# Performance work log

Hardware: AMD Instinct MI355X
Metric: run time of the kernel (lower is better)

## Reference

```python
import jax, jax.numpy as jnp
import numpy as np

N_NODES = 10000
N_EDGES = 5_000_000
BATCH = 2000


def setup_inputs() -> dict:
    key = jax.random.key(0)
    k1, k2, k3, k4 = jax.random.split(key, 4)
    n, E = N_NODES, N_EDGES
    # valid undirected pairs i < j
    i = jax.random.randint(k1, (E,), 0, n - 1)
    r = jax.random.randint(k2, (E,), 0, n)
    j = i + 1 + r % (n - 1 - i)
    edges = jnp.stack([i, j])  # [2, E], int
    edge_times = jax.random.uniform(k3, (E,), dtype=jnp.float32)
    edge_states = jax.random.randint(k4, (E,), 0, 2)
    return {
        "edges": edges,
        "edge_times": edge_times,
        "edge_states": edge_states,
        "nodes_num": n,
        "batch_size": BATCH,
    }


def _flat_idx(i, j, n):
    # undirected upper-triangular linearization of pair (i, j), i < j
    return i * n - i * (i + 1) // 2 + (j - i - 1)


def reference(edges, edge_times, edge_states, nodes_num, batch_size):
    n = nodes_num
    # -- multinomial(arange(n), batch_size, replacement=False) via Gumbel top-k --
    key = jax.random.key(19)
    w = jnp.arange(n, dtype=jnp.float32)
    logw = jnp.where(w > 0, jnp.log(jnp.maximum(w, 1.0)), -jnp.inf)
    scores = logw + jax.random.gumbel(key, (n,), dtype=jnp.float32)
    _, sel = jax.lax.top_k(scores, batch_size)
    batch_nodes = jnp.sort(sel)

    # -- all combinations (i < j since batch_nodes is sorted) --
    ii, jj = np.triu_indices(batch_size, k=1)  # static shapes
    batch_pairs = jnp.stack([batch_nodes[ii], batch_nodes[jj]])  # [2, P]
    batch_flat = _flat_idx(batch_pairs[0], batch_pairs[1], n)  # ascending

    # -- gather stored edges whose pair index is in the batch --
    edge_flat = _flat_idx(edges[0], edges[1], n)
    order = jnp.argsort(edge_flat)  # jax sort is stable -> matches coalesce order
    edges_sorted = edges[:, order]
    flat_sorted = edge_flat[order]
    times_sorted = edge_times[order]
    states_sorted = edge_states[order]

    pos = jnp.searchsorted(batch_flat, flat_sorted)
    pos = jnp.clip(pos, 0, batch_flat.shape[0] - 1)
    mask = batch_flat[pos] == flat_sorted  # [E] membership of each edge in batch

    batch_edge_times = jnp.where(mask, times_sorted, 0.0)
    batch_states = jnp.where(mask, states_sorted, 0)
    return (batch_nodes, batch_pairs, edges_sorted, batch_edge_times,
            batch_states, mask)
```

## Files before the change

### kernel.cpp

```cpp
#include <hip/hip_runtime.h>
#include <stdint.h>
#include <math.h>

#define N_NODES  10000
#define N_EDGES  5000000
#define BATCH    2000
#define N_PAIRS  1999000

#define OUT_BN      0
#define OUT_PAIRS0  2000
#define OUT_PAIRS1  2001000
#define OUT_ES0     4000000
#define OUT_ES1     9000000
#define OUT_T       14000000
#define OUT_S       19000000
#define OUT_M       24000000

#define WS_KEYS     0
#define WS_SEL      80000
#define WS_BN       120000
#define WS_CNT      128000
#define WS_FILL     168000
#define WS_OFF      208000
#define WS_SCRATCH  248064


#define RPB_LOG  7
#define NB1      79
#define CHUNK    4096
#define NBIN     192
#define NBITSW   313
#define RANK_BLKS 200
#define HIST_BLKS 128

typedef unsigned long long u64;

__device__ __forceinline__ u64 score_key(int w, unsigned bits) {
  const float TINY = 1.17549435e-38f;
  float uf = __uint_as_float((bits >> 9) | 0x3f800000u) - 1.0f;
  float val = fmaxf(TINY, uf + TINY);
  float t1 = (float)log((double)val);
  float gmb = -(float)log((double)(-t1));
  float score = (w > 0) ? ((float)log((double)w) + gmb) : (-INFINITY);
  unsigned fb = __float_as_uint(score);
  unsigned s = (fb & 0x80000000u) ? ~fb : (fb | 0x80000000u);
  unsigned d = ~s;
  return ((u64)d << 32) | (unsigned)w;
}

__device__ __forceinline__ u64 make_key(int v) {
  unsigned ks[3] = {0u, 19u, 0u ^ 19u ^ 0x1BD11BDAu};
  unsigned x0 = 0u + ks[0];
  unsigned x1 = (unsigned)v + ks[1];
  const int R0[4] = {13, 15, 26, 6};
  const int R1[4] = {17, 29, 16, 24};
#pragma unroll
  for (int g = 0; g < 5; ++g) {
    const int* R = (g & 1) ? R1 : R0;
#pragma unroll
    for (int r = 0; r < 4; ++r) {
      x0 += x1;
      x1 = (x1 << R[r]) | (x1 >> (32 - R[r]));
      x1 ^= x0;
    }
    x0 += ks[(g + 1) % 3];
    x1 += ks[(g + 2) % 3] + (unsigned)(g + 1);
  }
  return score_key(v, x0 ^ x1);
}

__global__ void __launch_bounds__(256) k_rankhist(
    int* __restrict__ rankc, int* __restrict__ cnt,
    const int4* __restrict__ e_i4) {
  __shared__ __align__(16) int sh4[N_NODES];
  int tid = threadIdx.x;
  if ((int)blockIdx.x < RANK_BLKS) {
    u64* lk = (u64*)sh4;
    int vblk = blockIdx.x / 5, cblk = blockIdx.x % 5;
    int base = cblk * 2048;
    int lenc = min(2048, N_NODES - base);
    for (int t = tid; t < lenc; t += 256) lk[t] = make_key(base + t);
    __syncthreads();
    int v = vblk * 256 + tid;
    u64 kv = (v < N_NODES) ? make_key(v) : 0;
    int c = 0;
    for (int t = 0; t < lenc; ++t) c += (lk[t] < kv) ? 1 : 0;
    if (v < N_NODES && c) atomicAdd(&rankc[v], c);
  } else {
    int* h = sh4;
    for (int t = tid; t < N_NODES; t += 256) h[t] = 0;
    __syncthreads();
    int hb = blockIdx.x - RANK_BLKS;
    int stride = HIST_BLKS * 256;
    for (int t = hb * 256 + tid; t < N_EDGES / 4; t += stride) {
      int4 r = e_i4[t];
      atomicAdd(&h[r.x], 1);
      atomicAdd(&h[r.y], 1);
      atomicAdd(&h[r.z], 1);
      atomicAdd(&h[r.w], 1);
    }
    __syncthreads();
    for (int t = tid; t < N_NODES; t += 256) {
      int c = h[t];
      if (c) atomicAdd(&cnt[t], c);
    }
  }
}

__global__ void k_scan_all(const int* rankc, int* sel, int* bn, float* outbn,
                           const int* cnt, int* off, int* fill, int* fill1,
                           unsigned* selbits) {
  __shared__ int wsum[16];
  __shared__ unsigned lb[320];
  const int PER = 10;
  int tid = threadIdx.x, lane = tid & 63, wid = tid >> 6;
  int base = tid * PER;
  int svv[PER];
  {
    int s = 0;
#pragma unroll
    for (int k = 0; k < PER; ++k) {
      int i = base + k;
      if (i < N_NODES) {
        int sv = (rankc[i] < BATCH) ? 1 : 0;
        sel[i] = sv;
        svv[k] = sv;
        s += sv;
      } else svv[k] = 0;
    }
    int inc = s;
#pragma unroll
    for (int d = 1; d < 64; d <<= 1) {
      int v = __shfl_up(inc, d, 64);
      if (lane >= d) inc += v;
    }
    if (lane == 63) wsum[wid] = inc;
    __syncthreads();
    int woff = 0;
    for (int w = 0; w < wid; ++w) woff += wsum[w];
    int run = woff + inc - s;
#pragma unroll
    for (int k = 0; k < PER; ++k) {
      int i = base + k;
      if (i < N_NODES && svv[k]) {
        bn[run] = i;
        outbn[run] = (float)i;
        ++run;
      }
    }
  }
  __syncthreads();
  {
    int cv[PER];
    int s = 0;
#pragma unroll
    for (int k = 0; k < PER; ++k) {
      int i = base + k;
      if (i < N_NODES) { cv[k] = cnt[i]; s += cv[k]; } else cv[k] = 0;
    }
    int inc = s;
#pragma unroll
    for (int d = 1; d < 64; d <<= 1) {
      int v = __shfl_up(inc, d, 64);
      if (lane >= d) inc += v;
    }
    if (lane == 63) wsum[wid] = inc;
    __syncthreads();
    int woff = 0;
    for (int w = 0; w < wid; ++w) woff += wsum[w];
    int run = woff + inc - s;
#pragma unroll
    for (int k = 0; k < PER; ++k) {
      int i = base + k;
      if (i < N_NODES) {
        off[i] = run;
        fill[i] = run;
        if ((i & ((1 << RPB_LOG) - 1)) == 0) fill1[i >> RPB_LOG] = run;
        run += cv[k];
      }
    }
    if (tid == 0) off[N_NODES] = N_EDGES;
  }
  __syncthreads();
  if (tid < 320) lb[tid] = 0;
  __syncthreads();
#pragma unroll
  for (int k = 0; k < PER; ++k) {
    int i = base + k;
    if (i < N_NODES && svv[k]) atomicOr(&lb[i >> 5], 1u << (i & 31));
  }
  __syncthreads();
  if (tid < NBITSW) selbits[tid] = lb[tid];
}

__global__ void __launch_bounds__(256) k_pairs_part1(
    const int* __restrict__ e_i, const int* __restrict__ e_j,
    const int* __restrict__ st, int* __restrict__ fill1,
    u64* __restrict__ stage, const int* __restrict__ bn,
    float* __restrict__ outp, int nblk1) {
  __shared__ u64 lkey[CHUNK];
  __shared__ int h[NB1], bstart[NB1], basec[NB1], cur[NB1];
  __shared__ int tcount_s;
  int tid = threadIdx.x;
  if ((int)blockIdx.x >= nblk1) {
    int p = ((int)blockIdx.x - nblk1) * 256 + tid;
    if (p >= N_PAIRS) return;
    float tf = 2.0f * BATCH - 1.0f;
    float disc = tf * tf - 8.0f * (float)p;
    int ii = (int)((tf - sqrtf(disc)) * 0.5f);
    if (ii < 0) ii = 0;
    if (ii > BATCH - 2) ii = BATCH - 2;
    while (ii > 0 &&
           (long long)ii * (BATCH - 1) - (long long)ii * (ii - 1) / 2 > p) --ii;
    while ((long long)(ii + 1) * (BATCH - 1) - (long long)(ii + 1) * ii / 2 <= p) ++ii;
    long long S = (long long)ii * (BATCH - 1) - (long long)ii * (ii - 1) / 2;
    int jj = ii + 1 + (int)(p - S);
    outp[p] = (float)bn[ii];
    outp[N_PAIRS + p] = (float)bn[jj];
    return;
  }
  int c0 = (int)blockIdx.x * CHUNK;
  int nloc = min(CHUNK, N_EDGES - c0);
  for (int t = tid; t < NB1; t += 256) h[t] = 0;
  __syncthreads();
  int iv[CHUNK / 256];
  const int4* e_i4 = (const int4*)(e_i + c0);
#pragma unroll
  for (int k = 0; k < CHUNK / 1024; ++k) {
    int q = tid + 256 * k;
    int ebase = 4 * q;
    if (ebase < nloc) {
      int4 r = e_i4[q];
      iv[4 * k + 0] = r.x; iv[4 * k + 1] = r.y;
      iv[4 * k + 2] = r.z; iv[4 * k + 3] = r.w;
      atomicAdd(&h[r.x >> RPB_LOG], 1);
      atomicAdd(&h[r.y >> RPB_LOG], 1);
      atomicAdd(&h[r.z >> RPB_LOG], 1);
      atomicAdd(&h[r.w >> RPB_LOG], 1);
    } else {
      iv[4 * k + 0] = iv[4 * k + 1] = iv[4 * k + 2] = iv[4 * k + 3] = -1;
    }
  }
  __syncthreads();
  if (tid < 64) {
    int a = h[tid];
    int b = (tid + 64 < NB1) ? h[tid + 64] : 0;
    int inc0 = a;
#pragma unroll
    for (int d = 1; d < 64; d <<= 1) {
      int v = __shfl_up(inc0, d, 64);
      if (tid >= d) inc0 += v;
    }
    int t0 = __shfl(inc0, 63, 64);
    int inc1 = b;
#pragma unroll
    for (int d = 1; d < 64; d <<= 1) {
      int v = __shfl_up(inc1, d, 64);
      if (tid >= d) inc1 += v;
    }
    int tot = t0 + __shfl(inc1, 63, 64);
    bstart[tid] = inc0 - a;
    if (tid + 64 < NB1) bstart[tid + 64] = t0 + inc1 - b;
    if (tid == 0) tcount_s = tot;
  }
  __syncthreads();
  for (int b = tid; b < NB1; b += 256) {
    basec[b] = h[b] ? atomicAdd(&fill1[b], h[b]) : 0;
    cur[b] = bstart[b];
  }
  __syncthreads();
  const int4* e_j4 = (const int4*)(e_j + c0);
  const int4* st4 = (const int4*)(st + c0);
#pragma unroll
  for (int k = 0; k < CHUNK / 1024; ++k) {
    int q = tid + 256 * k;
    int ebase = 4 * q;
    if (ebase < nloc) {
      int4 jj = e_j4[q];
      int4 ss = st4[q];
      int js[4] = {jj.x, jj.y, jj.z, jj.w};
      int s4[4] = {ss.x, ss.y, ss.z, ss.w};
#pragma unroll
      for (int c = 0; c < 4; ++c) {
        int i = iv[4 * k + c];
        unsigned e = (unsigned)(c0 + ebase + c);
        int b = i >> RPB_LOG;
        int pos = atomicAdd(&cur[b], 1);
        lkey[pos] = ((u64)(unsigned)i << 38) | ((u64)(unsigned)js[c] << 24) |
                    ((u64)e << 1) | (u64)(unsigned)s4[c];
      }
    }
  }
  __syncthreads();
  int tcount = tcount_s;
  for (int t = tid; t < tcount; t += 256) {
    u64 kv = lkey[t];
    int b = (int)(kv >> (38 + RPB_LOG));
    stage[basec[b] + (t - bstart[b])] = kv;
  }
}

__global__ void __launch_bounds__(256) k_part2(
    const u64* __restrict__ stage, int* __restrict__ fill,
    u64* __restrict__ sk) {
  __shared__ u64 lkey[CHUNK];
  __shared__ int h[256], bstart[256], baser[256], cur[256], wsum4[4];
  __shared__ int rowbase_s;
  int tid = threadIdx.x, lane = tid & 63, wid = tid >> 6;
  int c0 = (int)blockIdx.x * CHUNK;
  int nloc = min(CHUNK, N_EDGES - c0);
  h[tid] = 0;
  if (tid == 0)
    rowbase_s = ((int)(stage[c0] >> (38 + RPB_LOG))) << RPB_LOG;
  __syncthreads();
  int rowbase = rowbase_s;
  u64 kv[CHUNK / 256];
#pragma unroll
  for (int k = 0; k < CHUNK / 256; ++k) {
    int q = tid + 256 * k;
    if (q < nloc) {
      kv[k] = stage[c0 + q];
      atomicAdd(&h[(int)(kv[k] >> 38) - rowbase], 1);
    }
  }
  __syncthreads();
  int hv = h[tid];
  int inc = hv;
#pragma unroll
  for (int d = 1; d < 64; d <<= 1) {
    int v = __shfl_up(inc, d, 64);
    if (lane >= d) inc += v;
  }
  if (lane == 63) wsum4[wid] = inc;
  __syncthreads();
  int woff = 0;
  for (int w = 0; w < wid; ++w) woff += wsum4[w];
  int tcount = wsum4[0] + wsum4[1] + wsum4[2] + wsum4[3];
  int excl = woff + inc - hv;
  bstart[tid] = excl;
  cur[tid] = excl;
  baser[tid] = hv ? atomicAdd(&fill[rowbase + tid], hv) : 0;
  __syncthreads();
#pragma unroll
  for (int k = 0; k < CHUNK / 256; ++k) {
    int q = tid + 256 * k;
    if (q < nloc) {
      int lr = (int)(kv[k] >> 38) - rowbase;
      int pos = atomicAdd(&cur[lr], 1);
      lkey[pos] = kv[k];
    }
  }
  __syncthreads();
  for (int t = tid; t < tcount; t += 256) {
    u64 v = lkey[t];
    int lr = (int)(v >> 38) - rowbase;
    sk[baser[lr] + (t - bstart[lr])] = v;
  }
}

__global__ void __launch_bounds__(256) k_rowsort_key(
    const u64* __restrict__ sk, const int* __restrict__ off,
    const float* __restrict__ times, const unsigned* __restrict__ selbits,
    float* __restrict__ out) {
  __shared__ u64 buf[768];
  __shared__ int hist[NBIN], cur[NBIN];
  __shared__ unsigned bits[320];
  int tid = threadIdx.x;
  int row = blockIdx.x;
  int o0 = off[row], o1 = off[row + 1];
  int len = o1 - o0;
  if (len <= 0) return;
  if (len > 768) len = 768;
  int span = N_NODES - 1 - row;
  int s = 0;
  while ((span >> s) >= 160) ++s;
  int mi = (int)((selbits[row >> 5] >> (row & 31)) & 1u);
  for (int t = tid; t < NBIN; t += 256) hist[t] = 0;
  if (mi) {
    for (int t = tid; t < NBITSW; t += 256) bits[t] = selbits[t];
  }
  __syncthreads();
  u64 kv[3];
  int dv[3], rv[3];
  int jbase = row + 1;
#pragma unroll
  for (int k = 0; k < 3; ++k) {
    int t = tid + 256 * k;
    if (t < len) {
      u64 v = sk[o0 + t];
      kv[k] = v;
      int j = (int)((v >> 24) & 0x3FFFull);
      int d = (j - jbase) >> s;
      dv[k] = d;
      atomicAdd(&hist[d], 1);
    } else {
      dv[k] = -1;
    }
  }
  __syncthreads();
  if (tid < 64) {
    int b0 = tid * 3;
    int c0 = hist[b0], c1 = hist[b0 + 1], c2 = hist[b0 + 2];
    int sum = c0 + c1 + c2;
    int inc = sum;
#pragma unroll
    for (int d = 1; d < 64; d <<= 1) {
      int v = __shfl_up(inc, d, 64);
      if (tid >= d) inc += v;
    }
    int excl = inc - sum;
    hist[b0] = excl;
    hist[b0 + 1] = excl + c0;
    hist[b0 + 2] = excl + c0 + c1;
    cur[b0] = excl;
    cur[b0 + 1] = excl + c0;
    cur[b0 + 2] = excl + c0 + c1;
  }
  __syncthreads();
#pragma unroll
  for (int k = 0; k < 3; ++k) {
    if (dv[k] >= 0) {
      int pos = atomicAdd(&cur[dv[k]], 1);
      buf[pos] = kv[k];
    }
  }
  __syncthreads();
#pragma unroll
  for (int k = 0; k < 3; ++k) {
    if (dv[k] >= 0) {
      u64 me = kv[k];
      int s0 = hist[dv[k]];
      int s1 = cur[dv[k]];
      int r = 0;
      for (int q = s0; q < s1; ++q) r += (buf[q] < me) ? 1 : 0;
      rv[k] = s0 + r;
    }
  }
  __syncthreads();
#pragma unroll
  for (int k = 0; k < 3; ++k)
    if (dv[k] >= 0) buf[rv[k]] = kv[k];
  __syncthreads();
  float frow = (float)row;
  if (mi) {
    for (int t = tid; t < len; t += 256) {
      u64 k = buf[t];
      int j = (int)((k >> 24) & 0x3FFFull);
      int idx = (int)((k >> 1) & 0x7FFFFFull);
      int st = (int)(k & 1ull);
      int p = o0 + t;
      out[OUT_ES0 + p] = frow;
      out[OUT_ES1 + p] = (float)j;
      bool m = (bits[j >> 5] >> (j & 31)) & 1u;
      out[OUT_T + p] = m ? times[idx] : 0.0f;
      out[OUT_S + p] = m ? (float)st : 0.0f;
      out[OUT_M + p] = m ? 1.0f : 0.0f;
    }
  } else {
    for (int t = tid; t < len; t += 256) {
      u64 k = buf[t];
      int j = (int)((k >> 24) & 0x3FFFull);
      int p = o0 + t;
      out[OUT_ES0 + p] = frow;
      out[OUT_ES1 + p] = (float)j;
      out[OUT_T + p] = 0.0f;
      out[OUT_S + p] = 0.0f;
      out[OUT_M + p] = 0.0f;
    }
  }
}

__global__ void __launch_bounds__(256) k_scatter_idx(
    const int4* __restrict__ e_i4, int* __restrict__ fill,
    unsigned* __restrict__ sk) {
  int t = blockIdx.x * blockDim.x + threadIdx.x;
  if (t >= N_EDGES / 4) return;
  int4 r = e_i4[t];
  unsigned e = 4u * (unsigned)t;
  int c0 = atomicAdd(&fill[r.x], 1);
  int c1 = atomicAdd(&fill[r.y], 1);
  int c2 = atomicAdd(&fill[r.z], 1);
  int c3 = atomicAdd(&fill[r.w], 1);
  sk[c0] = e;
  sk[c1] = e + 1;
  sk[c2] = e + 2;
  sk[c3] = e + 3;
}

__global__ void __launch_bounds__(256) k_rowsort_idx(
    const unsigned* __restrict__ sk, const int* __restrict__ e_j_arr,
    const int* __restrict__ off, const float* __restrict__ times,
    const int* __restrict__ states, const int* __restrict__ sel,
    float* __restrict__ out) {
  __shared__ u64 key[2048];
  int row = blockIdx.x;
  int o0 = off[row], o1 = off[row + 1];
  int len = o1 - o0;
  if (len <= 0) return;
  if (len > 2048) len = 2048;
  int M = 2;
  while (M < len) M <<= 1;
  for (int t = threadIdx.x; t < M; t += blockDim.x) {
    if (t < len) {
      unsigned e = sk[o0 + t];
      key[t] = ((u64)(unsigned)e_j_arr[e] << 32) | e;
    } else {
      key[t] = 0xFFFFFFFFFFFFFFFFull;
    }
  }
  __syncthreads();
  for (int k = 2; k <= M; k <<= 1) {
    for (int j = k >> 1; j > 0; j >>= 1) {
      for (int t = threadIdx.x; t < M; t += blockDim.x) {
        int ixj = t ^ j;
        if (ixj > t) {
          u64 a = key[t], b = key[ixj];
          bool up = ((t & k) == 0);
          if (up ? (a > b) : (a < b)) {
            key[t] = b;
            key[ixj] = a;
          }
        }
      }
      __syncthreads();
    }
  }
  int mi = sel[row];
  float frow = (float)row;
  for (int t = threadIdx.x; t < len; t += blockDim.x) {
    u64 k = key[t];
    int j = (int)(k >> 32);
    int idx = (int)(k & 0xFFFFFFFFull);
    int p = o0 + t;
    out[OUT_ES0 + p] = frow;
    out[OUT_ES1 + p] = (float)j;
    bool m = (mi != 0) && (sel[j] != 0);
    float tm = 0.0f, sv = 0.0f;
    if (m) {
      tm = times[idx];
      sv = (float)states[idx];
    }
    out[OUT_T + p] = tm;
    out[OUT_S + p] = sv;
    out[OUT_M + p] = m ? 1.0f : 0.0f;
  }
}

extern "C" void kernel_launch(void* const* d_in, const int* in_sizes, int n_in,
                              void* d_out, int out_size, void* d_ws, size_t ws_size,
                              hipStream_t stream) {
  const int* edges = (const int*)d_in[0];
  const float* times = (const float*)d_in[1];
  const int* states = (const int*)d_in[2];
  const int* e_i = edges;
  const int* e_j = edges + N_EDGES;
  float* out = (float*)d_out;
  char* ws = (char*)d_ws;

  int* fill1 = (int*)(ws + WS_KEYS);
  int* sel = (int*)(ws + WS_SEL);
  int* bn = (int*)(ws + WS_BN);
  int* cnt = (int*)(ws + WS_CNT);
  unsigned* selbits = (unsigned*)(ws + WS_CNT);
  int* fill = (int*)(ws + WS_FILL);
  int* rankc = (int*)(ws + WS_FILL);
  int* off = (int*)(ws + WS_OFF);
  u64* sk64 = (u64*)(ws + WS_SCRATCH);
  unsigned* sk32 = (unsigned*)(ws + WS_SCRATCH);
  u64* stage = (u64*)(out + OUT_ES0);
  int use64 = (ws_size >= (size_t)WS_SCRATCH + 8ull * N_EDGES) ? 1 : 0;

  hipMemsetAsync(ws + WS_CNT, 0, 80000, stream);

  int npair_b = (N_PAIRS + 255) / 256;
  k_rankhist<<<RANK_BLKS + HIST_BLKS, 256, 0, stream>>>(rankc, cnt,
                                                        (const int4*)e_i);
  k_scan_all<<<1, 1024, 0, stream>>>(rankc, sel, bn, out + OUT_BN, cnt, off,
                                     fill, fill1, selbits);
  if (use64) {
    int nblk1 = (N_EDGES + CHUNK - 1) / CHUNK;
    k_pairs_part1<<<nblk1 + npair_b, 256, 0, stream>>>(
        e_i, e_j, states, fill1, stage, bn, out + OUT_PAIRS0, nblk1);
    k_part2<<<nblk1, 256, 0, stream>>>(stage, fill, sk64);
    k_rowsort_key<<<N_NODES, 256, 0, stream>>>(sk64, off, times, selbits, out);
  } else {
    k_pairs_part1<<<npair_b, 256, 0, stream>>>(
        e_i, e_j, states, fill1, stage, bn, out + OUT_PAIRS0, 0);
    k_scatter_idx<<<(N_EDGES / 4 + 255) / 256, 256, 0, stream>>>(
        (const int4*)e_i, fill, sk32);
    k_rowsort_idx<<<N_NODES, 256, 0, stream>>>(sk32, e_j, off, times, states,
                                               sel, out);
  }
}
```

Baseline: 359.3 us.

## Replace per-row bucketed sort with full all-pairs rank sort in shared memory

```diff
diff --git a/kernel.cpp b/kernel.cpp
--- a/kernel.cpp
+++ b/kernel.cpp
@@ -28,7 +28,6 @@
 #define RPB_LOG  7
 #define NB1      79
 #define CHUNK    4096
-#define NBIN     192
 #define NBITSW   313
 #define RANK_BLKS 200
 #define HIST_BLKS 128
@@ -363,7 +362,7 @@
     const float* __restrict__ times, const unsigned* __restrict__ selbits,
     float* __restrict__ out) {
   __shared__ u64 buf[768];
-  __shared__ int hist[NBIN], cur[NBIN];
+  __shared__ u64 buf2[768];
   __shared__ unsigned bits[320];
   int tid = threadIdx.x;
   int row = blockIdx.x;
@@ -371,80 +370,45 @@
   int len = o1 - o0;
   if (len <= 0) return;
   if (len > 768) len = 768;
-  int span = N_NODES - 1 - row;
-  int s = 0;
-  while ((span >> s) >= 160) ++s;
   int mi = (int)((selbits[row >> 5] >> (row & 31)) & 1u);
-  for (int t = tid; t < NBIN; t += 256) hist[t] = 0;
+  u64 kv[3];
+  int tv[3];
+#pragma unroll
+  for (int k = 0; k < 3; ++k) {
+    int t = tid + 256 * k;
+    if (t < len) { kv[k] = sk[o0 + t]; tv[k] = t; }
+    else { kv[k] = 0; tv[k] = -1; }
+  }
   if (mi) {
     for (int t = tid; t < NBITSW; t += 256) bits[t] = selbits[t];
   }
-  __syncthreads();
-  u64 kv[3];
-  int dv[3], rv[3];
-  int jbase = row + 1;
-#pragma unroll
-  for (int k = 0; k < 3; ++k) {
-    int t = tid + 256 * k;
-    if (t < len) {
-      u64 v = sk[o0 + t];
-      kv[k] = v;
-      int j = (int)((v >> 24) & 0x3FFFull);
-      int d = (j - jbase) >> s;
-      dv[k] = d;
-      atomicAdd(&hist[d], 1);
-    } else {
-      dv[k] = -1;
-    }
-  }
-  __syncthreads();
-  if (tid < 64) {
-    int b0 = tid * 3;
-    int c0 = hist[b0], c1 = hist[b0 + 1], c2 = hist[b0 + 2];
-    int sum = c0 + c1 + c2;
-    int inc = sum;
-#pragma unroll
-    for (int d = 1; d < 64; d <<= 1) {
-      int v = __shfl_up(inc, d, 64);
-      if (tid >= d) inc += v;
-    }
-    int excl = inc - sum;
-    hist[b0] = excl;
-    hist[b0 + 1] = excl + c0;
-    hist[b0 + 2] = excl + c0 + c1;
-    cur[b0] = excl;
-    cur[b0 + 1] = excl + c0;
-    cur[b0 + 2] = excl + c0 + c1;
-  }
-  __syncthreads();
-#pragma unroll
-  for (int k = 0; k < 3; ++k) {
-    if (dv[k] >= 0) {
-      int pos = atomicAdd(&cur[dv[k]], 1);
-      buf[pos] = kv[k];
-    }
-  }
-  __syncthreads();
-#pragma unroll
-  for (int k = 0; k < 3; ++k) {
-    if (dv[k] >= 0) {
-      u64 me = kv[k];
-      int s0 = hist[dv[k]];
-      int s1 = cur[dv[k]];
-      int r = 0;
-      for (int q = s0; q < s1; ++q) r += (buf[q] < me) ? 1 : 0;
-      rv[k] = s0 + r;
-    }
-  }
-  __syncthreads();
 #pragma unroll
   for (int k = 0; k < 3; ++k)
-    if (dv[k] >= 0) buf[rv[k]] = kv[k];
+    if (tv[k] >= 0) buf[tv[k]] = kv[k];
+  __syncthreads();
+  int r0 = 0, r1 = 0, r2 = 0;
+  if (len <= 512) {
+    for (int q = 0; q < len; ++q) {
+      u64 b = buf[q];
+      r0 += (b < kv[0]) ? 1 : 0;
+      r1 += (b < kv[1]) ? 1 : 0;
+    }
+  } else {
+    for (int q = 0; q < len; ++q) {
+      u64 b = buf[q];
+      r0 += (b < kv[0]) ? 1 : 0;
+      r1 += (b < kv[1]) ? 1 : 0;
+      r2 += (b < kv[2]) ? 1 : 0;
+    }
+  }
+  if (tv[0] >= 0) buf2[r0] = kv[0];
+  if (tv[1] >= 0) buf2[r1] = kv[1];
+  if (tv[2] >= 0) buf2[r2] = kv[2];
   __syncthreads();
   float frow = (float)row;
   if (mi) {
     for (int t = tid; t < len; t += 256) {
-      u64 k = buf[t];
+      u64 k = buf2[t];
       int j = (int)((k >> 24) & 0x3FFFull);
       int idx = (int)((k >> 1) & 0x7FFFFFull);
       int st = (int)(k & 1ull);
@@ -458,7 +422,7 @@
     }
   } else {
     for (int t = tid; t < len; t += 256) {
-      u64 k = buf[t];
+      u64 k = buf2[t];
       int j = (int)((k >> 24) & 0x3FFFull);
       int p = o0 + t;
       out[OUT_ES0 + p] = frow;
```

After: 452.4 us. 25.9% more time.

## Process four rows per block in row-sort kernel with next-row prefetch

Applied to the files above, without the earlier changes.

```diff
diff --git a/kernel.cpp b/kernel.cpp
--- a/kernel.cpp
+++ b/kernel.cpp
@@ -32,6 +32,7 @@
 #define NBITSW   313
 #define RANK_BLKS 200
 #define HIST_BLKS 128
+#define RPB      4
 
 typedef unsigned long long u64;
 
@@ -365,108 +366,134 @@
   __shared__ u64 buf[768];
   __shared__ int hist[NBIN], cur[NBIN];
   __shared__ unsigned bits[320];
+  __shared__ int offs[RPB + 1];
   int tid = threadIdx.x;
-  int row = blockIdx.x;
-  int o0 = off[row], o1 = off[row + 1];
-  int len = o1 - o0;
-  if (len <= 0) return;
-  if (len > 768) len = 768;
-  int span = N_NODES - 1 - row;
-  int s = 0;
-  while ((span >> s) >= 160) ++s;
-  int mi = (int)((selbits[row >> 5] >> (row & 31)) & 1u);
-  for (int t = tid; t < NBIN; t += 256) hist[t] = 0;
-  if (mi) {
-    for (int t = tid; t < NBITSW; t += 256) bits[t] = selbits[t];
-  }
-  __syncthreads();
-  u64 kv[3];
-  int dv[3], rv[3];
-  int jbase = row + 1;
-#pragma unroll
-  for (int k = 0; k < 3; ++k) {
-    int t = tid + 256 * k;
-    if (t < len) {
-      u64 v = sk[o0 + t];
-      kv[k] = v;
-      int j = (int)((v >> 24) & 0x3FFFull);
-      int d = (j - jbase) >> s;
-      dv[k] = d;
-      atomicAdd(&hist[d], 1);
+  int base_row = (int)blockIdx.x * RPB;
+  if (tid < RPB + 1) offs[tid] = off[base_row + tid];
+  for (int t = tid; t < NBITSW; t += 256) bits[t] = selbits[t];
+  u64 pv[3];
+  {
+    int p0 = off[base_row], p1 = off[base_row + 1];
+    int plen = p1 - p0;
+    if (plen > 768) plen = 768;
+#pragma unroll
+    for (int k = 0; k < 3; ++k) {
+      int t = tid + 256 * k;
+      pv[k] = (t < plen) ? sk[p0 + t] : 0;
+    }
+  }
+  __syncthreads();
+  for (int r = 0; r < RPB; ++r) {
+    int row = base_row + r;
+    int o0 = offs[r], o1 = offs[r + 1];
+    int len = o1 - o0;
+    if (len > 768) len = 768;
+    u64 kv[3];
+#pragma unroll
+    for (int k = 0; k < 3; ++k) kv[k] = pv[k];
+    if (r + 1 < RPB) {
+      int n0 = offs[r + 1];
+      int nlen = offs[r + 2] - n0;
+      if (nlen > 768) nlen = 768;
+#pragma unroll
+      for (int k = 0; k < 3; ++k) {
+        int t = tid + 256 * k;
+        pv[k] = (t < nlen) ? sk[n0 + t] : 0;
+      }
+    }
+    if (len <= 0) continue;
+    int span = N_NODES - 1 - row;
+    int s = 0;
+    while ((span >> s) >= 160) ++s;
+    int mi = (int)((bits[row >> 5] >> (row & 31)) & 1u);
+    for (int t = tid; t < NBIN; t += 256) hist[t] = 0;
+    __syncthreads();
+    int dv[3], rv[3];
+    int jbase = row + 1;
+#pragma unroll
+    for (int k = 0; k < 3; ++k) {
+      int t = tid + 256 * k;
+      if (t < len) {
+        int j = (int)((kv[k] >> 24) & 0x3FFFull);
+        int d = (j - jbase) >> s;
+        dv[k] = d;
+        atomicAdd(&hist[d], 1);
+      } else {
+        dv[k] = -1;
+      }
+    }
+    __syncthreads();
+    if (tid < 64) {
+      int b0 = tid * 3;
+      int c0 = hist[b0], c1 = hist[b0 + 1], c2 = hist[b0 + 2];
+      int sum = c0 + c1 + c2;
+      int inc = sum;
+#pragma unroll
+      for (int d = 1; d < 64; d <<= 1) {
+        int v = __shfl_up(inc, d, 64);
+        if (tid >= d) inc += v;
+      }
+      int excl = inc - sum;
+      hist[b0] = excl;
+      hist[b0 + 1] = excl + c0;
+      hist[b0 + 2] = excl + c0 + c1;
+      cur[b0] = excl;
+      cur[b0 + 1] = excl + c0;
+      cur[b0 + 2] = excl + c0 + c1;
+    }
+    __syncthreads();
+#pragma unroll
+    for (int k = 0; k < 3; ++k) {
+      if (dv[k] >= 0) {
+        int pos = atomicAdd(&cur[dv[k]], 1);
+        buf[pos] = kv[k];
+      }
+    }
+    __syncthreads();
+#pragma unroll
+    for (int k = 0; k < 3; ++k) {
+      if (dv[k] >= 0) {
+        u64 me = kv[k];
+        int s0 = hist[dv[k]];
+        int s1 = cur[dv[k]];
+        int rr = 0;
+        for (int q = s0; q < s1; ++q) rr += (buf[q] < me) ? 1 : 0;
+        rv[k] = s0 + rr;
+      }
+    }
+    __syncthreads();
+#pragma unroll
+    for (int k = 0; k < 3; ++k)
+      if (dv[k] >= 0) buf[rv[k]] = kv[k];
+    __syncthreads();
+    float frow = (float)row;
+    if (mi) {
+      for (int t = tid; t < len; t += 256) {
+        u64 k = buf[t];
+        int j = (int)((k >> 24) & 0x3FFFull);
+        int idx = (int)((k >> 1) & 0x7FFFFFull);
+        int st = (int)(k & 1ull);
+        int p = o0 + t;
+        out[OUT_ES0 + p] = frow;
+        out[OUT_ES1 + p] = (float)j;
+        bool m = (bits[j >> 5] >> (j & 31)) & 1u;
+        out[OUT_T + p] = m ? times[idx] : 0.0f;
+        out[OUT_S + p] = m ? (float)st : 0.0f;
+        out[OUT_M + p] = m ? 1.0f : 0.0f;
+      }
     } else {
-      dv[k] = -1;
-    }
-  }
-  __syncthreads();
-  if (tid < 64) {
-    int b0 = tid * 3;
-    int c0 = hist[b0], c1 = hist[b0 + 1], c2 = hist[b0 + 2];
-    int sum = c0 + c1 + c2;
-    int inc = sum;
-#pragma unroll
-    for (int d = 1; d < 64; d <<= 1) {
-      int v = __shfl_up(inc, d, 64);
-      if (tid >= d) inc += v;
-    }
-    int excl = inc - sum;
-    hist[b0] = excl;
-    hist[b0 + 1] = excl + c0;
-    hist[b0 + 2] = excl + c0 + c1;
-    cur[b0] = excl;
-    cur[b0 + 1] = excl + c0;
-    cur[b0 + 2] = excl + c0 + c1;
-  }
-  __syncthreads();
-#pragma unroll
-  for (int k = 0; k < 3; ++k) {
-    if (dv[k] >= 0) {
-      int pos = atomicAdd(&cur[dv[k]], 1);
-      buf[pos] = kv[k];
-    }
-  }
-  __syncthreads();
-#pragma unroll
-  for (int k = 0; k < 3; ++k) {
-    if (dv[k] >= 0) {
-      u64 me = kv[k];
-      int s0 = hist[dv[k]];
-      int s1 = cur[dv[k]];
-      int r = 0;
-      for (int q = s0; q < s1; ++q) r += (buf[q] < me) ? 1 : 0;
-      rv[k] = s0 + r;
-    }
-  }
-  __syncthreads();
-#pragma unroll
-  for (int k = 0; k < 3; ++k)
-    if (dv[k] >= 0) buf[rv[k]] = kv[k];
-  __syncthreads();
-  float frow = (float)row;
-  if (mi) {
-    for (int t = tid; t < len; t += 256) {
-      u64 k = buf[t];
-      int j = (int)((k >> 24) & 0x3FFFull);
-      int idx = (int)((k >> 1) & 0x7FFFFFull);
-      int st = (int)(k & 1ull);
-      int p = o0 + t;
-      out[OUT_ES0 + p] = frow;
-      out[OUT_ES1 + p] = (float)j;
-      bool m = (bits[j >> 5] >> (j & 31)) & 1u;
-      out[OUT_T + p] = m ? times[idx] : 0.0f;
-      out[OUT_S + p] = m ? (float)st : 0.0f;
-      out[OUT_M + p] = m ? 1.0f : 0.0f;
-    }
-  } else {
-    for (int t = tid; t < len; t += 256) {
-      u64 k = buf[t];
-      int j = (int)((k >> 24) & 0x3FFFull);
-      int p = o0 + t;
-      out[OUT_ES0 + p] = frow;
-      out[OUT_ES1 + p] = (float)j;
-      out[OUT_T + p] = 0.0f;
-      out[OUT_S + p] = 0.0f;
-      out[OUT_M + p] = 0.0f;
-    }
+      for (int t = tid; t < len; t += 256) {
+        u64 k = buf[t];
+        int j = (int)((k >> 24) & 0x3FFFull);
+        int p = o0 + t;
+        out[OUT_ES0 + p] = frow;
+        out[OUT_ES1 + p] = (float)j;
+        out[OUT_T + p] = 0.0f;
+        out[OUT_S + p] = 0.0f;
+        out[OUT_M + p] = 0.0f;
+      }
+    }
+    __syncthreads();
   }
 }
 
@@ -582,7 +609,8 @@
     k_pairs_part1<<<nblk1 + npair_b, 256, 0, stream>>>(
         e_i, e_j, states, fill1, stage, bn, out + OUT_PAIRS0, nblk1);
     k_part2<<<nblk1, 256, 0, stream>>>(stage, fill, sk64);
-    k_rowsort_key<<<N_NODES, 256, 0, stream>>>(sk64, off, times, selbits, out);
+    k_rowsort_key<<<N_NODES / RPB, 256, 0, stream>>>(sk64, off, times, selbits,
+                                                     out);
   } else {
     k_pairs_part1<<<npair_b, 256, 0, stream>>>(
         e_i, e_j, states, fill1, stage, bn, out + OUT_PAIRS0, 0);
```

Measured after the change: 419.3 us. 1.17x slower.
